# Kernel tuning notes

Measured on AMD Instinct MI355X. Metric: run time of the kernel, lower is better.

Reference implementation:

```python
import jax, jax.numpy as jnp
import numpy as np

C = 256
GROUPS = 32
HEADS = 4
EPS = 1e-5

def setup_inputs() -> dict:
    key = jax.random.key(0)
    ks = jax.random.split(key, 6)
    N, H, W = 4, 64, 64
    s = 1.0 / np.sqrt(C)
    return {
        "x": jax.random.normal(ks[0], (N, C, H, W), dtype=jnp.float32),
        "gamma": jnp.ones((C,), jnp.float32),
        "beta": jnp.zeros((C,), jnp.float32),
        "Wq": jax.random.normal(ks[1], (C, C), jnp.float32) * s,
        "Wk": jax.random.normal(ks[2], (C, C), jnp.float32) * s,
        "Wv": jax.random.normal(ks[3], (C, C), jnp.float32) * s,
        "Wp": jax.random.normal(ks[4], (C, C), jnp.float32) * s,
        "bp": jnp.zeros((C,), jnp.float32),
    }

def group_norm(x, gamma, beta):
    N, Cc, H, W = x.shape
    xg = x.reshape(N, GROUPS, Cc // GROUPS, H, W)
    mean = jnp.mean(xg, axis=(2, 3, 4), keepdims=True)
    var = jnp.var(xg, axis=(2, 3, 4), keepdims=True)
    xg = (xg - mean) * jax.lax.rsqrt(var + EPS)
    x = xg.reshape(N, Cc, H, W)
    return x * gamma[None, :, None, None] + beta[None, :, None, None]

def reference(x, gamma, beta, Wq, Wk, Wv, Wp, bp):
    N, Cc, H, W = x.shape
    dh = Cc // HEADS
    L = H * W
    xn = group_norm(x, gamma, beta)           # [N,C,H,W]
    xf = xn.reshape(N, Cc, L)                 # [N,C,L]
    # 1x1 convs == channel matmuls; split into heads: [N,heads,L,dh]
    def proj_heads(Wm):
        t = jnp.einsum('oc,ncl->nol', Wm, xf)
        return t.reshape(N, HEADS, dh, L).transpose(0, 1, 3, 2)
    q = proj_heads(Wq)
    k = proj_heads(Wk)
    v = proj_heads(Wv)
    scale = dh ** -0.5
    attn = jnp.einsum('nhld,nhmd->nhlm', q, k) * scale  # [N,heads,L,L]
    attn = jax.nn.softmax(attn, axis=-1)
    out = jnp.einsum('nhlm,nhmd->nhld', attn, v)        # [N,heads,L,dh]
    out = out.transpose(0, 1, 3, 2).reshape(N, Cc, L)   # [N,C,L]
    out = jnp.einsum('oc,ncl->nol', Wp, out) + bp[None, :, None]
    return out.reshape(N, Cc, H, W)
```

## Files before the change

kernel.cpp:

```cpp
#include <hip/hip_runtime.h>
#include <cstddef>
#include <cstdint>

#define NB 4
#define CC 256
#define LL 4096
#define NG 32
#define CPG 8
#define NH 4
#define DH 64
#define PSPLIT 4194304

static constexpr float EPSV  = 1e-5f;
static constexpr float SCALE_Q = 0.125f * 1.4426950408889634f;

typedef __attribute__((ext_vector_type(8))) short bf16x8;
typedef __attribute__((ext_vector_type(4))) float f32x4;
typedef _Float16 f16x8 __attribute__((ext_vector_type(8)));
typedef _Float16 f16x4 __attribute__((ext_vector_type(4)));
typedef __fp16  h16x2 __attribute__((ext_vector_type(2)));

__device__ __forceinline__ short f2bf(float f) {
  unsigned u = __float_as_uint(f);
  unsigned r = (u + 0x7fffu + ((u >> 16) & 1u)) >> 16;
  return (short)r;
}
__device__ __forceinline__ short f2h(float f) {
  union { _Float16 h; short s; } u;
  u.h = (_Float16)f;
  return u.s;
}
__device__ __forceinline__ int sw(int row, int chunk) {
  return row * 64 + ((chunk ^ (row & 7)) * 8);
}

__global__ __launch_bounds__(256) void gnstats_wcvt(
    const float* __restrict__ x, float* __restrict__ pstat,
    const float* __restrict__ Wq, const float* __restrict__ Wk,
    const float* __restrict__ Wv, const float* __restrict__ Wp,
    short* __restrict__ wdst) {
  __shared__ float r1[4], r2[4];
  const int blk = blockIdx.x;
  if (blk < 512) {
    const int grp = blk >> 2, qtr = blk & 3;
    const float* xp = x + (size_t)grp * CPG * LL + qtr * 1024 + threadIdx.x * 4;
    float s = 0.f, ss = 0.f;
    #pragma unroll
    for (int cc = 0; cc < 8; ++cc) {
      const float4 v = *(const float4*)(xp + (size_t)cc * LL);
      s  += v.x + v.y + v.z + v.w;
      ss += v.x * v.x + v.y * v.y + v.z * v.z + v.w * v.w;
    }
    #pragma unroll
    for (int off = 32; off; off >>= 1) {
      s  += __shfl_down(s, off);
      ss += __shfl_down(ss, off);
    }
    const int wid = threadIdx.x >> 6, lane = threadIdx.x & 63;
    if (lane == 0) { r1[wid] = s; r2[wid] = ss; }
    __syncthreads();
    if (threadIdx.x == 0) {
      float S = 0.f, SS = 0.f;
      #pragma unroll
      for (int w = 0; w < 4; ++w) { S += r1[w]; SS += r2[w]; }
      pstat[blk * 2]     = S;
      pstat[blk * 2 + 1] = SS;
    }
  } else {
    const int wblk = blk - 512;
    const int which = wblk >> 5;
    const float* src = (which == 0) ? Wq : (which == 1) ? Wk : (which == 2) ? Wv : Wp;
    const int base = (wblk & 31) * 2048 + threadIdx.x * 8;
    const float4 v0 = *(const float4*)(src + base);
    const float4 v1 = *(const float4*)(src + base + 4);
    short ob[8] __attribute__((aligned(16)));
    if (which < 3) {
      ob[0] = f2bf(v0.x); ob[1] = f2bf(v0.y); ob[2] = f2bf(v0.z); ob[3] = f2bf(v0.w);
      ob[4] = f2bf(v1.x); ob[5] = f2bf(v1.y); ob[6] = f2bf(v1.z); ob[7] = f2bf(v1.w);
    } else {
      ob[0] = f2h(v0.x); ob[1] = f2h(v0.y); ob[2] = f2h(v0.z); ob[3] = f2h(v0.w);
      ob[4] = f2h(v1.x); ob[5] = f2h(v1.y); ob[6] = f2h(v1.z); ob[7] = f2h(v1.w);
    }
    const int o = base >> 8, c = base & 255;
    const int dst = (((o >> 4) * 8 + (c >> 5)) * 64 + ((c >> 3) & 3) * 16 + (o & 15)) * 8;
    *(uint4*)(wdst + which * 65536 + dst) = *(const uint4*)ob;
  }
}

__global__ __launch_bounds__(256) void qkv_gemm(
    const float* __restrict__ x, const float* __restrict__ gamma,
    const float* __restrict__ beta, const float* __restrict__ pstat,
    const short* __restrict__ Wqb, const short* __restrict__ Wkb,
    const short* __restrict__ Wvb,
    short* __restrict__ Qt, short* __restrict__ Kt, _Float16* __restrict__ Vo) {
  __shared__ __align__(16) short smem[64 * 272];
  const int lt = blockIdx.y, ot2 = blockIdx.x;
  const int n = lt >> 6, l0 = (lt & 63) << 6;
  const int wave = threadIdx.x >> 6, lane = threadIdx.x & 63;
  const int lq = lane & 15, quad = lane >> 4;

  #pragma unroll
  for (int i = 0; i < 2; ++i) {
    const int u = threadIdx.x + i * 256;
    const int cc = u >> 4, l4 = u & 15;
    const int grp = n * NG + cc;
    float S = 0.f, SS = 0.f;
    #pragma unroll
    for (int w = 0; w < 4; ++w) {
      S  += pstat[(grp * 4 + w) * 2];
      SS += pstat[(grp * 4 + w) * 2 + 1];
    }
    const float mean = S / 32768.f;
    const float rstd = rsqrtf(SS / 32768.f - mean * mean + EPSV);
    const float* xp = x + (size_t)(n * CC + cc * CPG) * LL + l0 + l4 * 4;
    short ob[4][8] __attribute__((aligned(16)));
    #pragma unroll
    for (int j = 0; j < 8; ++j) {
      const float scl = rstd * gamma[cc * CPG + j];
      const float shf = beta[cc * CPG + j] - mean * scl;
      const float4 v = *(const float4*)(xp + (size_t)j * LL);
      ob[0][j] = f2bf(v.x * scl + shf);
      ob[1][j] = f2bf(v.y * scl + shf);
      ob[2][j] = f2bf(v.z * scl + shf);
      ob[3][j] = f2bf(v.w * scl + shf);
    }
    short* dst = smem + (l4 * 4) * 264 + cc * 8;
    #pragma unroll
    for (int jj = 0; jj < 4; ++jj)
      *(uint4*)(dst + jj * 264) = *(const uint4*)ob[jj];
  }
  __syncthreads();

  const int tb   = (ot2 * 8 + wave) * 8;
  const int loff = lane * 8;
  const short* xl = smem + lq * 264 + quad * 8;

  const f32x4 z = {0.f, 0.f, 0.f, 0.f};
  f32x4 aq[2][4] = {{z, z, z, z}, {z, z, z, z}};
  f32x4 ak[2][4] = {{z, z, z, z}, {z, z, z, z}};
  f32x4 av[2][4] = {{z, z, z, z}, {z, z, z, z}};

  #pragma unroll
  for (int c5 = 0; c5 < 8; ++c5) {
    const int c0 = c5 * 32;
    const bf16x8 fq0 = *(const bf16x8*)(Wqb + (tb + c5) * 512 + loff);
    const bf16x8 fq1 = *(const bf16x8*)(Wqb + (tb + 32 + c5) * 512 + loff);
    const bf16x8 fk0 = *(const bf16x8*)(Wkb + (tb + c5) * 512 + loff);
    const bf16x8 fk1 = *(const bf16x8*)(Wkb + (tb + 32 + c5) * 512 + loff);
    const bf16x8 fv0 = *(const bf16x8*)(Wvb + (tb + c5) * 512 + loff);
    const bf16x8 fv1 = *(const bf16x8*)(Wvb + (tb + 32 + c5) * 512 + loff);
    #pragma unroll
    for (int n0 = 0; n0 < 4; ++n0) {
      const bf16x8 fb = *(const bf16x8*)(xl + (n0 * 16) * 264 + c0);
      aq[0][n0] = __builtin_amdgcn_mfma_f32_16x16x32_bf16(fq0, fb, aq[0][n0], 0, 0, 0);
      aq[1][n0] = __builtin_amdgcn_mfma_f32_16x16x32_bf16(fq1, fb, aq[1][n0], 0, 0, 0);
      ak[0][n0] = __builtin_amdgcn_mfma_f32_16x16x32_bf16(fk0, fb, ak[0][n0], 0, 0, 0);
      ak[1][n0] = __builtin_amdgcn_mfma_f32_16x16x32_bf16(fk1, fb, ak[1][n0], 0, 0, 0);
      av[0][n0] = __builtin_amdgcn_mfma_f32_16x16x32_bf16(fv0, fb, av[0][n0], 0, 0, 0);
      av[1][n0] = __builtin_amdgcn_mfma_f32_16x16x32_bf16(fv1, fb, av[1][n0], 0, 0, 0);
    }
  }

  #pragma unroll
  for (int w = 0; w < 2; ++w) {
    const size_t hb = (size_t)(n * NH + ot2 * 2 + w);
    #pragma unroll
    for (int n0 = 0; n0 < 4; ++n0)
      #pragma unroll
      for (int r = 0; r < 4; ++r)
        Vo[(hb * DH + wave * 16 + quad * 4 + r) * LL + l0 + n0 * 16 + lq] =
            (_Float16)av[w][n0][r];
  }

  __syncthreads();
  short* qt_l = smem;
  short* kt_l = smem + 64 * 136;
  #pragma unroll
  for (int w = 0; w < 2; ++w)
    #pragma unroll
    for (int n0 = 0; n0 < 4; ++n0)
      #pragma unroll
      for (int r = 0; r < 4; ++r) {
        const int row = n0 * 16 + lq;
        const int col = w * 64 + wave * 16 + quad * 4 + r;
        qt_l[row * 136 + col] = f2bf(aq[w][n0][r] * SCALE_Q);
        kt_l[row * 136 + col] = f2bf(ak[w][n0][r]);
      }
  __syncthreads();
  #pragma unroll
  for (int i = 0; i < 4; ++i) {
    const int u = threadIdx.x + i * 256;
    const int row = u >> 4, ch16 = u & 15;
    const int h = ot2 * 2 + (ch16 >> 3);
    const int d0 = (ch16 & 7) * 8;
    const size_t hb = (size_t)(n * NH + h);
    *(uint4*)(Qt + (hb * LL + l0 + row) * DH + d0) = *(const uint4*)&qt_l[row * 136 + ch16 * 8];
    *(uint4*)(Kt + (hb * LL + l0 + row) * DH + d0) = *(const uint4*)&kt_l[row * 136 + ch16 * 8];
  }
}

__global__ __launch_bounds__(256, 2) void attn_mfma_kernel(
    const short* __restrict__ Qt, const short* __restrict__ Kt,
    const _Float16* __restrict__ Vb, _Float16* __restrict__ Opart,
    float* __restrict__ lpart) {
  __shared__ __align__(16) short    k_lds[2][64 * 64];
  __shared__ __align__(16) _Float16 v_lds[2][64 * 64];

  const int t = threadIdx.x;
  const int wave = t >> 6, lane = t & 63;
  const int lq = lane & 15, quad = lane >> 4;
  const int l0 = blockIdx.x * 256;
  const int h = blockIdx.y >> 1, split = blockIdx.y & 1;
  const int n = blockIdx.z;
  const int kbase = split * 2048;
  const int R = n * NH + h;
  const size_t hb = (size_t)R * (size_t)LL * DH;
  const short* const Kp = Kt + hb;
  const _Float16* const Vp = Vb + hb;

  const int qbase = l0 + wave * 64;
  bf16x8 qb[4][2];
  #pragma unroll
  for (int qf = 0; qf < 4; ++qf)
    #pragma unroll
    for (int c = 0; c < 2; ++c)
      qb[qf][c] = *(const bf16x8*)(Qt + hb + (size_t)(qbase + qf * 16 + lq) * DH + c * 32 + quad * 8);

  const f32x4 z = {0.f, 0.f, 0.f, 0.f};
  f32x4 o[4][4] = {{z, z, z, z}, {z, z, z, z}, {z, z, z, z}, {z, z, z, z}};
  f32x4 ol[4] = {z, z, z, z};

  f16x8 ones8;
  #pragma unroll
  for (int i = 0; i < 8; ++i) ones8[i] = (_Float16)1.0f;

  const int srow = t >> 3, sch = t & 7;
  const int vgo = 32 * (sch >> 2) + 4 * (sch & 3);

  {
    *(uint4*)&k_lds[0][sw(srow, sch)]      = *(const uint4*)(Kp + (size_t)(kbase + srow) * DH + sch * 8);
    *(uint4*)&k_lds[0][sw(32 + srow, sch)] = *(const uint4*)(Kp + (size_t)(kbase + 32 + srow) * DH + sch * 8);
    const _Float16* vg0 = Vp + (size_t)srow * LL + kbase + vgo;
    const _Float16* vg1 = Vp + (size_t)(32 + srow) * LL + kbase + vgo;
    uint2 a = *(const uint2*)vg0, b = *(const uint2*)(vg0 + 16);
    *(uint4*)&v_lds[0][sw(srow, sch)] = make_uint4(a.x, a.y, b.x, b.y);
    a = *(const uint2*)vg1; b = *(const uint2*)(vg1 + 16);
    *(uint4*)&v_lds[0][sw(32 + srow, sch)] = make_uint4(a.x, a.y, b.x, b.y);
  }
  __syncthreads();

  for (int kt = 0; kt < 32; ++kt) {
    const int cur = kt & 1;
    uint4 kpre[2]; uint2 vpre[4];
    if (kt < 31) {
      const int kpos = kbase + (kt + 1) * 64;
      kpre[0] = *(const uint4*)(Kp + (size_t)(kpos + srow) * DH + sch * 8);
      kpre[1] = *(const uint4*)(Kp + (size_t)(kpos + 32 + srow) * DH + sch * 8);
      const _Float16* vg0 = Vp + (size_t)srow * LL + kpos + vgo;
      const _Float16* vg1 = Vp + (size_t)(32 + srow) * LL + kpos + vgo;
      vpre[0] = *(const uint2*)vg0;
      vpre[1] = *(const uint2*)(vg0 + 16);
      vpre[2] = *(const uint2*)vg1;
      vpre[3] = *(const uint2*)(vg1 + 16);
    }
    const short* kb = k_lds[cur];
    const _Float16* vbuf = v_lds[cur];

    union PU { f16x4 h4[2]; f16x8 h8; } af[2][4];
    #pragma unroll
    for (int mf = 0; mf < 4; ++mf) {
      const bf16x8 ka0 = *(const bf16x8*)&kb[sw(mf * 16 + lq, quad)];
      const bf16x8 ka1 = *(const bf16x8*)&kb[sw(mf * 16 + lq, 4 + quad)];
      #pragma unroll
      for (int qf = 0; qf < 4; ++qf) {
        f32x4 zz = {0.f, 0.f, 0.f, 0.f};
        zz = __builtin_amdgcn_mfma_f32_16x16x32_bf16(ka0, qb[qf][0], zz, 0, 0, 0);
        zz = __builtin_amdgcn_mfma_f32_16x16x32_bf16(ka1, qb[qf][1], zz, 0, 0, 0);
        union { h16x2 h2[2]; f16x4 h4; } u;
        u.h2[0] = __builtin_amdgcn_cvt_pkrtz(__builtin_amdgcn_exp2f(zz[0]),
                                             __builtin_amdgcn_exp2f(zz[1]));
        u.h2[1] = __builtin_amdgcn_cvt_pkrtz(__builtin_amdgcn_exp2f(zz[2]),
                                             __builtin_amdgcn_exp2f(zz[3]));
        af[mf >> 1][qf].h4[mf & 1] = u.h4;
      }
    }

    #pragma unroll
    for (int qf = 0; qf < 4; ++qf) {
      ol[qf] = __builtin_amdgcn_mfma_f32_16x16x32_f16(af[0][qf].h8, ones8, ol[qf], 0, 0, 0);
      ol[qf] = __builtin_amdgcn_mfma_f32_16x16x32_f16(af[1][qf].h8, ones8, ol[qf], 0, 0, 0);
    }

    #pragma unroll
    for (int df = 0; df < 4; ++df)
      #pragma unroll
      for (int cc = 0; cc < 2; ++cc) {
        const f16x8 vb8 = *(const f16x8*)&vbuf[sw(df * 16 + lq, cc * 4 + quad)];
        #pragma unroll
        for (int qf = 0; qf < 4; ++qf)
          o[qf][df] = __builtin_amdgcn_mfma_f32_16x16x32_f16(af[cc][qf].h8, vb8, o[qf][df], 0, 0, 0);
      }

    if (kt < 31) {
      const int nxt = 1 - cur;
      *(uint4*)&k_lds[nxt][sw(srow, sch)]      = kpre[0];
      *(uint4*)&k_lds[nxt][sw(32 + srow, sch)] = kpre[1];
      *(uint4*)&v_lds[nxt][sw(srow, sch)]      = make_uint4(vpre[0].x, vpre[0].y, vpre[1].x, vpre[1].y);
      *(uint4*)&v_lds[nxt][sw(32 + srow, sch)] = make_uint4(vpre[2].x, vpre[2].y, vpre[3].x, vpre[3].y);
      __syncthreads();
    }
  }

  const size_t pb = ((size_t)split * 16 + R) * (size_t)LL * DH;
  #pragma unroll
  for (int qf = 0; qf < 4; ++qf) {
    if (lq == 0) {
      #pragma unroll
      for (int r = 0; r < 4; ++r)
        lpart[((size_t)split * 16 + R) * LL + qbase + qf * 16 + quad * 4 + r] = ol[qf][r];
    }
    #pragma unroll
    for (int df = 0; df < 4; ++df)
      #pragma unroll
      for (int r = 0; r < 4; ++r) {
        const int q = qbase + qf * 16 + quad * 4 + r;
        Opart[pb + (size_t)q * DH + df * 16 + lq] = (_Float16)o[qf][df][r];
      }
  }
}

__global__ __launch_bounds__(256) void proj_gemm(
    const _Float16* __restrict__ Opart, const float* __restrict__ lpart,
    const _Float16* __restrict__ Wpf, const float* __restrict__ bp,
    float* __restrict__ out) {
  __shared__ __align__(16) _Float16 fb_lds[2][64 * 64];
  const int lt = blockIdx.y, ot2 = blockIdx.x;
  const int n = lt >> 6, l0 = (lt & 63) << 6;
  const int wave = threadIdx.x >> 6, lane = threadIdx.x & 63;
  const int lq = lane & 15, quad = lane >> 4;
  const int t = threadIdx.x;
  const int qr = t >> 3, ch = t & 7;

  const int tb   = (ot2 * 8 + wave) * 8;
  const int loff = lane * 8;

  auto stage = [&](int buf, int h) {
    const _Float16* Op = Opart + ((size_t)(n * NH + h) * LL + l0) * DH;
    #pragma unroll
    for (int half = 0; half < 2; ++half) {
      const int q = half * 32 + qr;
      const size_t rr = (size_t)(n * NH + h) * LL + l0 + q;
      const _Float16 il = (_Float16)(1.0f / (lpart[rr] + lpart[rr + 16 * (size_t)LL]));
      const size_t e = (size_t)q * DH + ch * 8;
      const f16x8 b0 = *(const f16x8*)(Op + e);
      const f16x8 b1 = *(const f16x8*)(Op + e + (size_t)PSPLIT);
      f16x8 sc8;
      #pragma unroll
      for (int i = 0; i < 8; ++i) sc8[i] = il;
      const f16x8 fbn = (b0 + b1) * sc8;
      *(f16x8*)&fb_lds[buf][sw(q, ch)] = fbn;
    }
  };

  stage(0, 0);
  __syncthreads();

  const f32x4 z = {0.f, 0.f, 0.f, 0.f};
  f32x4 acc[2][4] = {{z, z, z, z}, {z, z, z, z}};
  for (int h = 0; h < NH; ++h) {
    const int cur = h & 1;
    f16x8 pre[2];
    if (h < NH - 1) {
      const _Float16* Op = Opart + ((size_t)(n * NH + h + 1) * LL + l0) * DH;
      #pragma unroll
      for (int half = 0; half < 2; ++half) {
        const int q = half * 32 + qr;
        const size_t rr = (size_t)(n * NH + h + 1) * LL + l0 + q;
        const _Float16 il = (_Float16)(1.0f / (lpart[rr] + lpart[rr + 16 * (size_t)LL]));
        const size_t e = (size_t)q * DH + ch * 8;
        const f16x8 b0 = *(const f16x8*)(Op + e);
        const f16x8 b1 = *(const f16x8*)(Op + e + (size_t)PSPLIT);
        f16x8 sc8;
        #pragma unroll
        for (int i = 0; i < 8; ++i) sc8[i] = il;
        pre[half] = (b0 + b1) * sc8;
      }
    }
    #pragma unroll
    for (int cw = 0; cw < 2; ++cw) {
      const int c5 = 2 * h + cw;
      const int c_idx = cw * 4 + quad;
      const f16x8 fa0 = *(const f16x8*)(Wpf + (tb + c5) * 512 + loff);
      const f16x8 fa1 = *(const f16x8*)(Wpf + (tb + 32 + c5) * 512 + loff);
      #pragma unroll
      for (int n0 = 0; n0 < 4; ++n0) {
        const f16x8 fb = *(const f16x8*)&fb_lds[cur][sw(n0 * 16 + lq, c_idx)];
        acc[0][n0] = __builtin_amdgcn_mfma_f32_16x16x32_f16(fa0, fb, acc[0][n0], 0, 0, 0);
        acc[1][n0] = __builtin_amdgcn_mfma_f32_16x16x32_f16(fa1, fb, acc[1][n0], 0, 0, 0);
      }
    }
    if (h < NH - 1) {
      #pragma unroll
      for (int half = 0; half < 2; ++half)
        *(f16x8*)&fb_lds[cur ^ 1][sw(half * 32 + qr, ch)] = pre[half];
      __syncthreads();
    }
  }

  #pragma unroll
  for (int w = 0; w < 2; ++w)
    #pragma unroll
    for (int r = 0; r < 4; ++r) {
      const int oo = ot2 * 128 + w * 64 + wave * 16 + quad * 4 + r;
      const float bias = bp[oo];
      #pragma unroll
      for (int n0 = 0; n0 < 4; ++n0)
        out[((size_t)n * CC + oo) * LL + l0 + n0 * 16 + lq] = acc[w][n0][r] + bias;
    }
}

extern "C" void kernel_launch(void* const* d_in, const int* in_sizes, int n_in,
                              void* d_out, int out_size, void* d_ws, size_t ws_size,
                              hipStream_t stream) {
  const float* x     = (const float*)d_in[0];
  const float* gamma = (const float*)d_in[1];
  const float* beta  = (const float*)d_in[2];
  const float* Wq    = (const float*)d_in[3];
  const float* Wk    = (const float*)d_in[4];
  const float* Wv    = (const float*)d_in[5];
  const float* Wp    = (const float*)d_in[6];
  const float* bp    = (const float*)d_in[7];
  float* out = (float*)d_out;

  const size_t S = (size_t)NB * CC * LL;
  short*     Qt  = (short*)d_ws;
  short*     Kt  = Qt + S;
  _Float16*  Vo  = (_Float16*)(Kt + S);
  short*     Wb  = (short*)(Vo + S);
  _Float16*  Opart = (_Float16*)(Wb + 4 * 65536);
  float*     lpart = (float*)(Opart + 2 * (size_t)PSPLIT);
  float*     pstat = lpart + 2 * 16 * (size_t)LL;

  gnstats_wcvt<<<640,                 256, 0, stream>>>(x, pstat, Wq, Wk, Wv, Wp, Wb);
  qkv_gemm   <<<dim3(2, 256),         256, 0, stream>>>(x, gamma, beta, pstat,
                 Wb, Wb + 65536, Wb + 131072, Qt, Kt, Vo);
  attn_mfma_kernel<<<dim3(LL/256, NH*2, NB), 256, 0, stream>>>(Qt, Kt, Vo, Opart, lpart);
  proj_gemm  <<<dim3(2, 256),         256, 0, stream>>>(Opart, lpart,
                 (const _Float16*)(Wb + 196608), bp, out);
}
```

Before: 171.5 us.

## Halve GEMM spatial tile to 32 and store V pre-permuted for contiguous loads

The QKV and projection GEMM kernels now process 32 spatial positions per block instead of 64, doubling the grid so more blocks run at once and LDS per block shrinks. The QKV kernel also writes V in a permuted position order, so the attention kernel can load V tiles with single 16-byte loads instead of split 8-byte gathers. The tradeoff is that each block reuses the weight fragments across fewer positions, so weight reads per output rise, and the attention MMA must agree with the new V ordering.

```diff
diff --git a/kernel.cpp b/kernel.cpp
--- a/kernel.cpp
+++ b/kernel.cpp
@@ -93,16 +93,14 @@
     const short* __restrict__ Wqb, const short* __restrict__ Wkb,
     const short* __restrict__ Wvb,
     short* __restrict__ Qt, short* __restrict__ Kt, _Float16* __restrict__ Vo) {
-  __shared__ __align__(16) short smem[64 * 272];
+  __shared__ __align__(16) short smem[64 * 136];
   const int lt = blockIdx.y, ot2 = blockIdx.x;
-  const int n = lt >> 6, l0 = (lt & 63) << 6;
+  const int n = lt >> 7, l0 = (lt & 127) << 5;
   const int wave = threadIdx.x >> 6, lane = threadIdx.x & 63;
   const int lq = lane & 15, quad = lane >> 4;
 
-  #pragma unroll
-  for (int i = 0; i < 2; ++i) {
-    const int u = threadIdx.x + i * 256;
-    const int cc = u >> 4, l4 = u & 15;
+  {
+    const int cc = threadIdx.x >> 3, l8 = threadIdx.x & 7;
     const int grp = n * NG + cc;
     float S = 0.f, SS = 0.f;
     #pragma unroll
@@ -112,7 +110,7 @@
     }
     const float mean = S / 32768.f;
     const float rstd = rsqrtf(SS / 32768.f - mean * mean + EPSV);
-    const float* xp = x + (size_t)(n * CC + cc * CPG) * LL + l0 + l4 * 4;
+    const float* xp = x + (size_t)(n * CC + cc * CPG) * LL + l0 + l8 * 4;
     short ob[4][8] __attribute__((aligned(16)));
     #pragma unroll
     for (int j = 0; j < 8; ++j) {
@@ -124,7 +122,7 @@
       ob[2][j] = f2bf(v.z * scl + shf);
       ob[3][j] = f2bf(v.w * scl + shf);
     }
-    short* dst = smem + (l4 * 4) * 264 + cc * 8;
+    short* dst = smem + (l8 * 4) * 264 + cc * 8;
     #pragma unroll
     for (int jj = 0; jj < 4; ++jj)
       *(uint4*)(dst + jj * 264) = *(const uint4*)ob[jj];
@@ -136,9 +134,9 @@
   const short* xl = smem + lq * 264 + quad * 8;
 
   const f32x4 z = {0.f, 0.f, 0.f, 0.f};
-  f32x4 aq[2][4] = {{z, z, z, z}, {z, z, z, z}};
-  f32x4 ak[2][4] = {{z, z, z, z}, {z, z, z, z}};
-  f32x4 av[2][4] = {{z, z, z, z}, {z, z, z, z}};
+  f32x4 aq[2][2] = {{z, z}, {z, z}};
+  f32x4 ak[2][2] = {{z, z}, {z, z}};
+  f32x4 av[2][2] = {{z, z}, {z, z}};
 
   #pragma unroll
   for (int c5 = 0; c5 < 8; ++c5) {
@@ -150,7 +148,7 @@
     const bf16x8 fv0 = *(const bf16x8*)(Wvb + (tb + c5) * 512 + loff);
     const bf16x8 fv1 = *(const bf16x8*)(Wvb + (tb + 32 + c5) * 512 + loff);
     #pragma unroll
-    for (int n0 = 0; n0 < 4; ++n0) {
+    for (int n0 = 0; n0 < 2; ++n0) {
       const bf16x8 fb = *(const bf16x8*)(xl + (n0 * 16) * 264 + c0);
       aq[0][n0] = __builtin_amdgcn_mfma_f32_16x16x32_bf16(fq0, fb, aq[0][n0], 0, 0, 0);
       aq[1][n0] = __builtin_amdgcn_mfma_f32_16x16x32_bf16(fq1, fb, aq[1][n0], 0, 0, 0);
@@ -165,20 +163,21 @@
   for (int w = 0; w < 2; ++w) {
     const size_t hb = (size_t)(n * NH + ot2 * 2 + w);
     #pragma unroll
-    for (int n0 = 0; n0 < 4; ++n0)
+    for (int n0 = 0; n0 < 2; ++n0) {
+      const int pos = l0 + 8 * (lq >> 2) + 4 * n0 + (lq & 3);
       #pragma unroll
       for (int r = 0; r < 4; ++r)
-        Vo[(hb * DH + wave * 16 + quad * 4 + r) * LL + l0 + n0 * 16 + lq] =
-            (_Float16)av[w][n0][r];
+        Vo[(hb * DH + wave * 16 + quad * 4 + r) * LL + pos] = (_Float16)av[w][n0][r];
+    }
   }
 
   __syncthreads();
   short* qt_l = smem;
-  short* kt_l = smem + 64 * 136;
+  short* kt_l = smem + 32 * 136;
   #pragma unroll
   for (int w = 0; w < 2; ++w)
     #pragma unroll
-    for (int n0 = 0; n0 < 4; ++n0)
+    for (int n0 = 0; n0 < 2; ++n0)
       #pragma unroll
       for (int r = 0; r < 4; ++r) {
         const int row = n0 * 16 + lq;
@@ -188,7 +187,7 @@
       }
   __syncthreads();
   #pragma unroll
-  for (int i = 0; i < 4; ++i) {
+  for (int i = 0; i < 2; ++i) {
     const int u = threadIdx.x + i * 256;
     const int row = u >> 4, ch16 = u & 15;
     const int h = ot2 * 2 + (ch16 >> 3);
@@ -235,33 +234,24 @@
   for (int i = 0; i < 8; ++i) ones8[i] = (_Float16)1.0f;
 
   const int srow = t >> 3, sch = t & 7;
-  const int vgo = 32 * (sch >> 2) + 4 * (sch & 3);
 
   {
     *(uint4*)&k_lds[0][sw(srow, sch)]      = *(const uint4*)(Kp + (size_t)(kbase + srow) * DH + sch * 8);
     *(uint4*)&k_lds[0][sw(32 + srow, sch)] = *(const uint4*)(Kp + (size_t)(kbase + 32 + srow) * DH + sch * 8);
-    const _Float16* vg0 = Vp + (size_t)srow * LL + kbase + vgo;
-    const _Float16* vg1 = Vp + (size_t)(32 + srow) * LL + kbase + vgo;
-    uint2 a = *(const uint2*)vg0, b = *(const uint2*)(vg0 + 16);
-    *(uint4*)&v_lds[0][sw(srow, sch)] = make_uint4(a.x, a.y, b.x, b.y);
-    a = *(const uint2*)vg1; b = *(const uint2*)(vg1 + 16);
-    *(uint4*)&v_lds[0][sw(32 + srow, sch)] = make_uint4(a.x, a.y, b.x, b.y);
+    *(uint4*)&v_lds[0][sw(srow, sch)]      = *(const uint4*)(Vp + (size_t)srow * LL + kbase + sch * 8);
+    *(uint4*)&v_lds[0][sw(32 + srow, sch)] = *(const uint4*)(Vp + (size_t)(32 + srow) * LL + kbase + sch * 8);
   }
   __syncthreads();
 
   for (int kt = 0; kt < 32; ++kt) {
     const int cur = kt & 1;
-    uint4 kpre[2]; uint2 vpre[4];
+    uint4 kpre[2], vpre[2];
     if (kt < 31) {
       const int kpos = kbase + (kt + 1) * 64;
       kpre[0] = *(const uint4*)(Kp + (size_t)(kpos + srow) * DH + sch * 8);
       kpre[1] = *(const uint4*)(Kp + (size_t)(kpos + 32 + srow) * DH + sch * 8);
-      const _Float16* vg0 = Vp + (size_t)srow * LL + kpos + vgo;
-      const _Float16* vg1 = Vp + (size_t)(32 + srow) * LL + kpos + vgo;
-      vpre[0] = *(const uint2*)vg0;
-      vpre[1] = *(const uint2*)(vg0 + 16);
-      vpre[2] = *(const uint2*)vg1;
-      vpre[3] = *(const uint2*)(vg1 + 16);
+      vpre[0] = *(const uint4*)(Vp + (size_t)srow * LL + kpos + sch * 8);
+      vpre[1] = *(const uint4*)(Vp + (size_t)(32 + srow) * LL + kpos + sch * 8);
     }
     const short* kb = k_lds[cur];
     const _Float16* vbuf = v_lds[cur];
@@ -305,8 +295,8 @@
       const int nxt = 1 - cur;
       *(uint4*)&k_lds[nxt][sw(srow, sch)]      = kpre[0];
       *(uint4*)&k_lds[nxt][sw(32 + srow, sch)] = kpre[1];
-      *(uint4*)&v_lds[nxt][sw(srow, sch)]      = make_uint4(vpre[0].x, vpre[0].y, vpre[1].x, vpre[1].y);
-      *(uint4*)&v_lds[nxt][sw(32 + srow, sch)] = make_uint4(vpre[2].x, vpre[2].y, vpre[3].x, vpre[3].y);
+      *(uint4*)&v_lds[nxt][sw(srow, sch)]      = vpre[0];
+      *(uint4*)&v_lds[nxt][sw(32 + srow, sch)] = vpre[1];
       __syncthreads();
     }
   }
@@ -333,9 +323,9 @@
     const _Float16* __restrict__ Opart, const float* __restrict__ lpart,
     const _Float16* __restrict__ Wpf, const float* __restrict__ bp,
     float* __restrict__ out) {
-  __shared__ __align__(16) _Float16 fb_lds[2][64 * 64];
+  __shared__ __align__(16) _Float16 fb_lds[2][32 * 64];
   const int lt = blockIdx.y, ot2 = blockIdx.x;
-  const int n = lt >> 6, l0 = (lt & 63) << 6;
+  const int n = lt >> 7, l0 = (lt & 127) << 5;
   const int wave = threadIdx.x >> 6, lane = threadIdx.x & 63;
   const int lq = lane & 15, quad = lane >> 4;
   const int t = threadIdx.x;
@@ -344,48 +334,32 @@
   const int tb   = (ot2 * 8 + wave) * 8;
   const int loff = lane * 8;
 
-  auto stage = [&](int buf, int h) {
+  auto stage_load = [&](int h, f16x8& dst) {
     const _Float16* Op = Opart + ((size_t)(n * NH + h) * LL + l0) * DH;
-    #pragma unroll
-    for (int half = 0; half < 2; ++half) {
-      const int q = half * 32 + qr;
-      const size_t rr = (size_t)(n * NH + h) * LL + l0 + q;
-      const _Float16 il = (_Float16)(1.0f / (lpart[rr] + lpart[rr + 16 * (size_t)LL]));
-      const size_t e = (size_t)q * DH + ch * 8;
-      const f16x8 b0 = *(const f16x8*)(Op + e);
-      const f16x8 b1 = *(const f16x8*)(Op + e + (size_t)PSPLIT);
-      f16x8 sc8;
-      #pragma unroll
-      for (int i = 0; i < 8; ++i) sc8[i] = il;
-      const f16x8 fbn = (b0 + b1) * sc8;
-      *(f16x8*)&fb_lds[buf][sw(q, ch)] = fbn;
-    }
+    const size_t rr = (size_t)(n * NH + h) * LL + l0 + qr;
+    const _Float16 il = (_Float16)(1.0f / (lpart[rr] + lpart[rr + 16 * (size_t)LL]));
+    const size_t e = (size_t)qr * DH + ch * 8;
+    const f16x8 b0 = *(const f16x8*)(Op + e);
+    const f16x8 b1 = *(const f16x8*)(Op + e + (size_t)PSPLIT);
+    f16x8 sc8;
+    #pragma unroll
+    for (int i = 0; i < 8; ++i) sc8[i] = il;
+    dst = (b0 + b1) * sc8;
   };
 
-  stage(0, 0);
+  {
+    f16x8 f0;
+    stage_load(0, f0);
+    *(f16x8*)&fb_lds[0][sw(qr, ch)] = f0;
+  }
   __syncthreads();
 
   const f32x4 z = {0.f, 0.f, 0.f, 0.f};
-  f32x4 acc[2][4] = {{z, z, z, z}, {z, z, z, z}};
+  f32x4 acc[2][2] = {{z, z}, {z, z}};
   for (int h = 0; h < NH; ++h) {
     const int cur = h & 1;
-    f16x8 pre[2];
-    if (h < NH - 1) {
-      const _Float16* Op = Opart + ((size_t)(n * NH + h + 1) * LL + l0) * DH;
-      #pragma unroll
-      for (int half = 0; half < 2; ++half) {
-        const int q = half * 32 + qr;
-        const size_t rr = (size_t)(n * NH + h + 1) * LL + l0 + q;
-        const _Float16 il = (_Float16)(1.0f / (lpart[rr] + lpart[rr + 16 * (size_t)LL]));
-        const size_t e = (size_t)q * DH + ch * 8;
-        const f16x8 b0 = *(const f16x8*)(Op + e);
-        const f16x8 b1 = *(const f16x8*)(Op + e + (size_t)PSPLIT);
-        f16x8 sc8;
-        #pragma unroll
-        for (int i = 0; i < 8; ++i) sc8[i] = il;
-        pre[half] = (b0 + b1) * sc8;
-      }
-    }
+    f16x8 pre;
+    if (h < NH - 1) stage_load(h + 1, pre);
     #pragma unroll
     for (int cw = 0; cw < 2; ++cw) {
       const int c5 = 2 * h + cw;
@@ -393,16 +367,14 @@
       const f16x8 fa0 = *(const f16x8*)(Wpf + (tb + c5) * 512 + loff);
       const f16x8 fa1 = *(const f16x8*)(Wpf + (tb + 32 + c5) * 512 + loff);
       #pragma unroll
-      for (int n0 = 0; n0 < 4; ++n0) {
+      for (int n0 = 0; n0 < 2; ++n0) {
         const f16x8 fb = *(const f16x8*)&fb_lds[cur][sw(n0 * 16 + lq, c_idx)];
         acc[0][n0] = __builtin_amdgcn_mfma_f32_16x16x32_f16(fa0, fb, acc[0][n0], 0, 0, 0);
         acc[1][n0] = __builtin_amdgcn_mfma_f32_16x16x32_f16(fa1, fb, acc[1][n0], 0, 0, 0);
       }
     }
     if (h < NH - 1) {
-      #pragma unroll
-      for (int half = 0; half < 2; ++half)
-        *(f16x8*)&fb_lds[cur ^ 1][sw(half * 32 + qr, ch)] = pre[half];
+      *(f16x8*)&fb_lds[cur ^ 1][sw(qr, ch)] = pre;
       __syncthreads();
     }
   }
@@ -414,7 +386,7 @@
       const int oo = ot2 * 128 + w * 64 + wave * 16 + quad * 4 + r;
       const float bias = bp[oo];
       #pragma unroll
-      for (int n0 = 0; n0 < 4; ++n0)
+      for (int n0 = 0; n0 < 2; ++n0)
         out[((size_t)n * CC + oo) * LL + l0 + n0 * 16 + lq] = acc[w][n0][r] + bias;
     }
 }
@@ -442,9 +414,9 @@
   float*     pstat = lpart + 2 * 16 * (size_t)LL;
 
   gnstats_wcvt<<<640,                 256, 0, stream>>>(x, pstat, Wq, Wk, Wv, Wp, Wb);
-  qkv_gemm   <<<dim3(2, 256),         256, 0, stream>>>(x, gamma, beta, pstat,
+  qkv_gemm   <<<dim3(2, 512),         256, 0, stream>>>(x, gamma, beta, pstat,
                  Wb, Wb + 65536, Wb + 131072, Qt, Kt, Vo);
   attn_mfma_kernel<<<dim3(LL/256, NH*2, NB), 256, 0, stream>>>(Qt, Kt, Vo, Opart, lpart);
-  proj_gemm  <<<dim3(2, 256),         256, 0, stream>>>(Opart, lpart,
+  proj_gemm  <<<dim3(2, 512),         256, 0, stream>>>(Opart, lpart,
                  (const _Float16*)(Wb + 196608), bp, out);
 }
```

Result: no change. 172.3 us (+0.5%).
